# Optimization experiments

Measured on AMD Instinct MI355X. Metric: run time of the kernel, lower is better.

The kernel has to match this reference:

```python
import jax, jax.numpy as jnp
import numpy as np

N_HEAD = 4
GROUPS = 32
EPS = 1e-5


def _group_norm(x, w, b):
    B, C, H, W = x.shape
    g = x.reshape(B, GROUPS, C // GROUPS, H, W)
    mu = g.mean(axis=(2, 3, 4), keepdims=True)
    var = ((g - mu) ** 2).mean(axis=(2, 3, 4), keepdims=True)
    g = (g - mu) * jax.lax.rsqrt(var + EPS)
    return g.reshape(B, C, H, W) * w[None, :, None, None] + b[None, :, None, None]


def _l2norm(x):
    # F.normalize(x, dim=-1): x / max(||x||_2, 1e-12)
    n = jnp.sqrt(jnp.sum(x * x, axis=-1, keepdims=True))
    return x / jnp.maximum(n, 1e-12)


def _masked_softmax(attn, kk):
    # topk indices -> scatter 1s -> masked softmax (faithful to torch scatter_ path)
    idx = jax.lax.top_k(attn, kk)[1]                      # [B,H,c,kk]
    mask = jax.nn.one_hot(idx, attn.shape[-1], dtype=attn.dtype).sum(-2)  # [B,H,c,c]
    return jax.nn.softmax(jnp.where(mask > 0, attn, -jnp.inf), axis=-1)


def setup_inputs() -> dict:
    key = jax.random.key(0)
    ks = jax.random.split(key, 8)
    B, C, H, W = 4, 256, 128, 128
    x = jax.random.normal(ks[0], (B, C, H, W), jnp.float32)
    gn_w = 1.0 + 0.02 * jax.random.normal(ks[1], (C,), jnp.float32)
    gn_b = 0.02 * jax.random.normal(ks[2], (C,), jnp.float32)
    w_qkv = jax.random.normal(ks[3], (3 * C, C), jnp.float32) / np.sqrt(C).astype(np.float32)
    w_dw = jax.random.normal(ks[4], (3 * C, 1, 3, 3), jnp.float32) / 3.0
    w_out = jax.random.normal(ks[5], (C, C), jnp.float32) / np.sqrt(C).astype(np.float32)
    b_out = 0.01 * jax.random.normal(ks[6], (C,), jnp.float32)
    temperature = jnp.ones((N_HEAD, 1, 1), jnp.float32)
    attn_w = jnp.full((4,), 0.2, jnp.float32)  # attn1..attn4 combine weights
    return dict(x=x, gn_w=gn_w, gn_b=gn_b, w_qkv=w_qkv, w_dw=w_dw,
                w_out=w_out, b_out=b_out, temperature=temperature, attn_w=attn_w)


def reference(x, gn_w, gn_b, w_qkv, w_dw, w_out, b_out, temperature, attn_w):
    B, C, H, W = x.shape
    c = C // N_HEAD
    xn = _group_norm(x, gn_w, gn_b)
    # 1x1 conv (no bias)
    qkv = jnp.einsum('oi,bihw->bohw', w_qkv, xn)
    # 3x3 depthwise conv, padding=1, groups=3C, no bias
    qkv = jax.lax.conv_general_dilated(
        qkv, w_dw, window_strides=(1, 1), padding=((1, 1), (1, 1)),
        feature_group_count=3 * C,
        dimension_numbers=('NCHW', 'OIHW', 'NCHW'))
    q, k, v = jnp.split(qkv, 3, axis=1)
    # b (head c) h w -> b head c (h w)
    q = q.reshape(B, N_HEAD, c, H * W)
    k = k.reshape(B, N_HEAD, c, H * W)
    v = v.reshape(B, N_HEAD, c, H * W)
    q = _l2norm(q)
    k = _l2norm(k)
    # FFT cross-correlation attention (fftshift over ALL axes, as torch default)
    q_fft = jnp.fft.fftshift(jnp.fft.rfft2(q))   # [B,H,c,HW//2+1] complex
    k_fft = jnp.fft.fftshift(jnp.fft.rfft2(k))
    attn = jnp.einsum('bhcf,bhdf->bhcd', q_fft, k_fft) * temperature  # complex [B,H,c,c]
    attn = jnp.fft.irfft2(jnp.fft.ifftshift(attn), s=(c, c))          # real [B,H,c,c]
    ks_list = [c // 2, (c * 2) // 3, (c * 3) // 4, (c * 4) // 5]
    out = None
    for i, kk in enumerate(ks_list):
        a = _masked_softmax(attn, kk)
        o = jnp.einsum('bhcd,bhds->bhcs', a, v) * attn_w[i]
        out = o if out is None else out + o
    out = out.reshape(B, C, H, W)
    out = jnp.einsum('oi,bihw->bohw', w_out, out) + b_out[None, :, None, None]
    return out
```

## Files before the change

### kernel.cpp

```cpp
#include <hip/hip_runtime.h>
#include <math.h>

#define NC 256
#define CH3 768
#define HWSZ 16384

typedef __attribute__((ext_vector_type(8))) short short8;
typedef __attribute__((ext_vector_type(4))) float f32x4;
typedef __attribute__((ext_vector_type(4))) unsigned int u32x4;

static const size_t OFF_TW1   = 0;
static const size_t OFF_TW2   = 32768;
static const size_t OFF_HM    = 65536;
static const size_t OFF_SCALE = 65600;
static const size_t OFF_SHIFT = 66624;
static const size_t OFF_PACK  = 67648;
static const size_t OFF_AW    = 182336;
static const size_t OFF_GNP   = 444480;
static const size_t SHARED_END= 446528;

static const size_t R_QKV  = 0;
static const size_t R_SCR  = 12582912;
static const size_t R_H    = 25165824;
static const size_t R_PP   = 29360128;
static const size_t R_RP   = 30408704;
static const size_t R_ATTN = 31457280;
static const size_t R_ACOMB= 31473664;
static const size_t R_PS   = 31490048;
static const size_t R_RS   = 31506432;
static const size_t R_DWP  = 31522816;
static const size_t R_SSUM = 31532032;
static const size_t R_SALT = 31532800;
static const size_t R_SSQ  = 31533568;
static const size_t RSTRIDE= 31534336;
static const size_t HNOFF  = 8388608;

#define TDA_RH 0
#define TDA_RL 8192
#define TDA_IH 16384
#define TDA_IL 24576
#define ETA_RH 32768
#define ETA_RL 40960
#define ETA_IH 49152
#define ETA_IL 57344
#define STB_RH 65536
#define STB_RL 73728
#define STB_IH 81920
#define STB_IL 90112
#define STB_NIH 98304
#define STB_NIL 106496

#define AWQ_H 0
#define AWQ_L 98304
#define AWO_H 196608
#define AWO_L 229376

__device__ inline unsigned short b16rn(float x){
  unsigned u = __float_as_uint(x);
  return (unsigned short)((u + 0x7FFFu + ((u>>16)&1u)) >> 16);
}
__device__ inline unsigned int pk_hi(float x, float y){
  return (__float_as_uint(x)>>16) | (__float_as_uint(y) & 0xFFFF0000u);
}
__device__ inline unsigned int pk_lo(float x, float y){
  float xl = x - __uint_as_float(__float_as_uint(x) & 0xFFFF0000u);
  float yl = y - __uint_as_float(__float_as_uint(y) & 0xFFFF0000u);
  return (unsigned)b16rn(xl) | ((unsigned)b16rn(yl)<<16);
}
__device__ inline short8 ld8g(const unsigned int* p){ return *(const short8*)p; }
__device__ inline short8 ld8s(const unsigned short* p){ return *(const short8*)p; }
__device__ inline void wr_split(unsigned short* H, unsigned short* L, size_t o, float v){
  unsigned u = __float_as_uint(v);
  H[o] = (unsigned short)(u >> 16);
  L[o] = b16rn(v - __uint_as_float(u & 0xFFFF0000u));
}

__global__ __launch_bounds__(256) void init_tables_k(float* __restrict__ ws){
  int idx = blockIdx.x*256 + threadIdx.x;
  float2* tw1 = (float2*)(ws + OFF_TW1);
  float2* tw2 = (float2*)(ws + OFF_TW2);
  unsigned int* pk = (unsigned int*)(ws + OFF_PACK);
  const double P2 = 6.283185307179586476925286766559005;
  int m = idx >> 7, k = idx & 127;
  double a2 = P2 * (double)(m*k) / 16384.0;
  tw1[idx] = make_float2((float)cos(a2), (float)(-sin(a2)));
  tw2[idx] = make_float2((float)cos(a2), (float)( sin(a2)));
  if (idx < 64){
    double acc = 0.0;
    for (int v = 1; v < 32; v++) acc += sin(P2 * (double)((v*idx) & 63) / 64.0);
    ws[OFF_HM + idx] = (float)(-acc / 32.0);
  }
  if (idx < 8192){
    int r = idx >> 6, kp = idx & 63;
    int k0 = 2*kp, k1 = 2*kp+1;
    double a0 = P2 * (double)((r*k0) & 127) / 128.0;
    double a1 = P2 * (double)((r*k1) & 127) / 128.0;
    float c0 = (float)cos(a0), c1 = (float)cos(a1);
    float s0 = (float)sin(a0), s1 = (float)sin(a1);
    pk[TDA_RH + idx] = pk_hi(c0, c1);  pk[TDA_RL + idx] = pk_lo(c0, c1);
    pk[TDA_IH + idx] = pk_hi(-s0,-s1); pk[TDA_IL + idx] = pk_lo(-s0,-s1);
    pk[ETA_RH + idx] = pk_hi(c0, c1);  pk[ETA_RL + idx] = pk_lo(c0, c1);
    pk[ETA_IH + idx] = pk_hi(s0, s1);  pk[ETA_IL + idx] = pk_lo(s0, s1);
    float sr0, si0, sr1, si1;
    {
      int d0 = (r - k0) & 127, d1 = (r - k1) & 127;
      if (d0 == 0){ sr0 = 64.f; si0 = 0.f; }
      else if ((d0 & 1) == 0){ sr0 = 0.f; si0 = 0.f; }
      else { double th = 3.1415926535897932384626 * (double)d0 / 128.0;
             sr0 = 1.f; si0 = (float)(cos(th)/sin(th)); }
      if (d1 == 0){ sr1 = 64.f; si1 = 0.f; }
      else if ((d1 & 1) == 0){ sr1 = 0.f; si1 = 0.f; }
      else { double th = 3.1415926535897932384626 * (double)d1 / 128.0;
             sr1 = 1.f; si1 = (float)(cos(th)/sin(th)); }
    }
    pk[STB_RH + idx]  = pk_hi(sr0, sr1);  pk[STB_RL + idx]  = pk_lo(sr0, sr1);
    pk[STB_IH + idx]  = pk_hi(si0, si1);  pk[STB_IL + idx]  = pk_lo(si0, si1);
    pk[STB_NIH + idx] = pk_hi(-si0,-si1); pk[STB_NIL + idx] = pk_lo(-si0,-si1);
  }
}

__global__ __launch_bounds__(256) void wpack_k(const float* __restrict__ wqkv, const float* __restrict__ wout,
                                               unsigned int* __restrict__ aw){
  int id = blockIdx.x*256 + threadIdx.x;
  int row = id >> 7, kp = id & 127;
  if (row < CH3){
    float v0 = wqkv[row*256 + 2*kp], v1 = wqkv[row*256 + 2*kp + 1];
    aw[AWQ_H + row*128 + kp] = pk_hi(v0, v1);
    aw[AWQ_L + row*128 + kp] = pk_lo(v0, v1);
  } else {
    int r2 = row - CH3;
    float v0 = wout[r2*256 + 2*kp], v1 = wout[r2*256 + 2*kp + 1];
    aw[AWO_H + r2*128 + kp] = pk_hi(v0, v1);
    aw[AWO_L + r2*128 + kp] = pk_lo(v0, v1);
  }
}

__global__ __launch_bounds__(256) void gn_part_k(const float* __restrict__ x, float2* __restrict__ part){
  int id = blockIdx.x;
  const float4* p = (const float4*)(x + (size_t)id*HWSZ);
  int tid = threadIdx.x;
  float s = 0.f, sq = 0.f;
  #pragma unroll
  for (int i = 0; i < 16; i++){
    float4 v = p[tid + i*256];
    s  += v.x+v.y+v.z+v.w;
    sq += v.x*v.x+v.y*v.y+v.z*v.z+v.w*v.w;
  }
  __shared__ float r1[256], r2[256];
  r1[tid]=s; r2[tid]=sq; __syncthreads();
  for (int off=128; off; off>>=1){
    if (tid<off){ r1[tid]+=r1[tid+off]; r2[tid]+=r2[tid+off]; }
    __syncthreads();
  }
  if (tid==0) part[id] = make_float2(r1[0], r2[0]);
}
__global__ __launch_bounds__(128) void gn_fin_k(const float2* __restrict__ part, const float* __restrict__ gw,
                                                const float* __restrict__ gb, float* __restrict__ scale,
                                                float* __restrict__ shift){
  int bg = threadIdx.x;
  int b = bg >> 5, g = bg & 31;
  float s = 0.f, sq = 0.f;
  #pragma unroll
  for (int i = 0; i < 8; i++){
    float2 v = part[b*NC + g*8 + i];
    s += v.x; sq += v.y;
  }
  const float n = 8.0f*HWSZ;
  float mu = s/n, var = sq/n - mu*mu;
  float rs = rsqrtf(var + 1e-5f);
  for (int i = 0; i < 8; i++){
    int ch = g*8 + i;
    float sc = rs * gw[ch];
    scale[b*NC + ch] = sc;
    shift[b*NC + ch] = gb[ch] - mu*sc;
  }
}

__global__ __launch_bounds__(256) void packx_k(const float* __restrict__ xbase, const float* __restrict__ scale,
                                               const float* __restrict__ shift, float* __restrict__ R0,
                                               size_t rstride){
  int bz = blockIdx.z;
  const float* xb = xbase + (size_t)bz*NC*HWSZ;
  const float* sc = scale + bz*NC;
  const float* sh = shift + bz*NC;
  unsigned int* BqH = (unsigned int*)(R0 + (size_t)bz*rstride + R_H);
  unsigned int* BqL = BqH + 2097152;
  int kb = blockIdx.y;
  int n = blockIdx.x*256 + threadIdx.x;
  float v[8];
  #pragma unroll
  for (int c = 0; c < 8; c++){
    int ch = kb*8 + c;
    v[c] = xb[(size_t)ch*HWSZ + n]*sc[ch] + sh[ch];
  }
  u32x4 h, l;
  #pragma unroll
  for (int q = 0; q < 4; q++){
    h[q] = pk_hi(v[2*q], v[2*q+1]);
    l[q] = pk_lo(v[2*q], v[2*q+1]);
  }
  *(u32x4*)&BqH[((size_t)kb*HWSZ + n)*4] = h;
  *(u32x4*)&BqL[((size_t)kb*HWSZ + n)*4] = l;
}

__global__ __launch_bounds__(256) void gemm_pk(const unsigned int* __restrict__ Ah, const unsigned int* __restrict__ Al,
                                               const unsigned int* __restrict__ Bh0, const unsigned int* __restrict__ Bl0,
                                               const float* __restrict__ bias, float* __restrict__ C0,
                                               size_t bstride, size_t cstride){
  const unsigned int* Bh = Bh0 + (size_t)blockIdx.z*bstride;
  const unsigned int* Bl = Bl0 + (size_t)blockIdx.z*bstride;
  float* C = C0 + (size_t)blockIdx.z*cstride;
  int tid = threadIdx.x;
  int lane = tid & 63, wid = tid >> 6;
  int m0 = blockIdx.y*128, n0 = blockIdx.x*128;
  int wr = (wid>>1)*64, wc = (wid&1)*64;
  int lr = lane & 15, lk = lane >> 4;
  f32x4 acc[4][4] = {};
  size_t aoff[4], boff[4];
  #pragma unroll
  for (int i=0;i<4;i++) aoff[i] = (size_t)(m0 + wr + i*16 + lr)*128 + lk*4;
  #pragma unroll
  for (int j=0;j<4;j++) boff[j] = ((size_t)lk*HWSZ + n0 + wc + j*16 + lr)*4;
  short8 aH[2][4], aL[2][4], bH[2][4], bL[2][4];
  #pragma unroll
  for (int i=0;i<4;i++){ aH[0][i] = ld8g(Ah + aoff[i]); aL[0][i] = ld8g(Al + aoff[i]); }
  #pragma unroll
  for (int j=0;j<4;j++){ bH[0][j] = ld8g(Bh + boff[j]); bL[0][j] = ld8g(Bl + boff[j]); }
  #pragma unroll
  for (int kt = 0; kt < 8; kt++){
    int cur = kt & 1, nxt = cur ^ 1;
    if (kt < 7){
      size_t da = (size_t)(kt+1)*16;
      size_t db = (size_t)(kt+1)*4*HWSZ*4;
      #pragma unroll
      for (int i=0;i<4;i++){ aH[nxt][i] = ld8g(Ah + aoff[i] + da); aL[nxt][i] = ld8g(Al + aoff[i] + da); }
      #pragma unroll
      for (int j=0;j<4;j++){ bH[nxt][j] = ld8g(Bh + boff[j] + db); bL[nxt][j] = ld8g(Bl + boff[j] + db); }
    }
    #pragma unroll
    for (int i=0;i<4;i++)
      #pragma unroll
      for (int j=0;j<4;j++){
        acc[i][j] = __builtin_amdgcn_mfma_f32_16x16x32_bf16(aH[cur][i], bH[cur][j], acc[i][j], 0,0,0);
        acc[i][j] = __builtin_amdgcn_mfma_f32_16x16x32_bf16(aH[cur][i], bL[cur][j], acc[i][j], 0,0,0);
        acc[i][j] = __builtin_amdgcn_mfma_f32_16x16x32_bf16(aL[cur][i], bH[cur][j], acc[i][j], 0,0,0);
      }
  }
  #pragma unroll
  for (int i=0;i<4;i++){
    #pragma unroll
    for (int e=0;e<4;e++){
      int row = m0 + wr + i*16 + lk*4 + e;
      float bb = bias ? bias[row] : 0.0f;
      #pragma unroll
      for (int j=0;j<4;j++)
        C[(size_t)row*HWSZ + n0 + wc + j*16 + lr] = acc[i][j][e] + bb;
    }
  }
}

__global__ __launch_bounds__(256) void dwconv_tiled_k(float* __restrict__ R0, size_t rstride,
                                                      const float* __restrict__ wdw){
  float* Rb = R0 + (size_t)blockIdx.y*rstride;
  int blk = blockIdx.x;
  int ch = blk >> 2, sl = blk & 3;
  int h0 = sl*32;
  const float* in = Rb + R_SCR + (size_t)ch*HWSZ;
  float* part = Rb + R_DWP;
  float w[9];
  #pragma unroll
  for (int i=0;i<9;i++) w[i] = wdw[ch*9+i];
  __shared__ float tile[34][132];
  __shared__ float r0[256], r1[256], r2[256];
  int tid = threadIdx.x;
  #pragma unroll
  for (int i = 0; i < 5; i++){
    int id = tid + i*256;
    if (id < 1088){
      int r = id >> 5, c4 = id & 31;
      int gh = h0 - 1 + r;
      float4 v = (gh >= 0 && gh < 128) ? *(const float4*)&in[gh*128 + c4*4]
                                       : make_float4(0.f,0.f,0.f,0.f);
      *(float4*)&tile[r][c4*4] = v;
    }
  }
  __syncthreads();
  float s=0.f, sa=0.f, sq=0.f;
  #pragma unroll
  for (int it=0; it<4; it++){
    int idx = it*256 + tid;
    int lh = idx >> 5;
    int xq = idx & 31;
    int xb4 = xq*4;
    float o[4];
    #pragma unroll
    for (int e=0;e<4;e++){
      int xw = xb4 + e;
      float acc = 0.f;
      #pragma unroll
      for (int ky=0; ky<3; ky++){
        const float* tr = &tile[lh+ky][xw];
        if (xw > 0)   acc += tr[-1]*w[ky*3+0];
                      acc += tr[ 0]*w[ky*3+1];
        if (xw < 127) acc += tr[ 1]*w[ky*3+2];
      }
      o[e] = acc;
      s += acc; sq += acc*acc;
      sa += (e & 1) ? -acc : acc;
    }
    int sbase = (h0+lh)*128 + xb4;
    if (ch < 256){
      unsigned short* QHo = (unsigned short*)(Rb + R_QKV);
      unsigned short* QLo = (unsigned short*)(Rb + R_QKV + 2097152);
      size_t ro = (size_t)ch*HWSZ;
      #pragma unroll
      for (int e=0;e<4;e++){
        int sf = (16384 - (sbase+e)) & 16383;
        wr_split(QHo, QLo, ro + sf, o[e]);
      }
    } else if (ch < 512){
      unsigned short* KHo = (unsigned short*)(Rb + R_H);
      unsigned short* KLo = (unsigned short*)(Rb + R_H + 2097152);
      size_t ro = (size_t)(ch-256)*HWSZ;
      #pragma unroll
      for (int e=0;e<4;e++)
        wr_split(KHo, KLo, ro + sbase+e, o[e]);
    } else {
      *(float4*)&(Rb + R_QKV + (size_t)ch*HWSZ)[sbase] = make_float4(o[0],o[1],o[2],o[3]);
    }
  }
  r0[tid]=s; r1[tid]=sa; r2[tid]=sq; __syncthreads();
  for (int off=128; off; off>>=1){
    if (tid<off){ r0[tid]+=r0[tid+off]; r1[tid]+=r1[tid+off]; r2[tid]+=r2[tid+off]; }
    __syncthreads();
  }
  if (tid==0){ part[blk]=r0[0]; part[3072+blk]=r1[0]; part[6144+blk]=r2[0]; }
}

__global__ __launch_bounds__(256) void fft1_mfma_k(const float* __restrict__ ws, float* __restrict__ R0,
                                                   size_t rstride){
  float* Rb = R0 + (size_t)blockIdx.y*rstride;
  const unsigned short* KH = (const unsigned short*)(Rb + R_H);
  const unsigned short* KL = (const unsigned short*)(Rb + R_H + 2097152);
  float2* Tc = (float2*)(Rb + R_SCR);
  const unsigned int* PK = (const unsigned int*)(ws + OFF_PACK);
  const float2* tw1 = (const float2*)(ws + OFF_TW1);
  __shared__ unsigned int Bth[128][20], Btl[128][20];
  int tid = threadIdx.x;
  int lane = tid & 63, wid = tid >> 6;
  int wr = (wid>>1)*64, wc = (wid&1)*64;
  int lr = lane & 15, lk = lane >> 4;
  int row = blockIdx.x;
  f32x4 aR[4][4] = {}, aI[4][4] = {};
  int bc = tid & 127, grp = tid >> 7;
  for (int kt = 0; kt < 4; kt++){
    #pragma unroll
    for (int p=0;p<8;p++){
      int kp = grp*8 + p;
      int a = kt*32 + 2*kp;
      size_t o0 = (size_t)row*HWSZ + a*128 + bc;
      Bth[bc][kp] = (unsigned)KH[o0] | ((unsigned)KH[o0+128] << 16);
      Btl[bc][kp] = (unsigned)KL[o0] | ((unsigned)KL[o0+128] << 16);
    }
    __syncthreads();
    short8 bh[4], bl[4];
    #pragma unroll
    for (int j=0;j<4;j++){
      bh[j] = *(const short8*)&Bth[wc + j*16 + lr][lk*4];
      bl[j] = *(const short8*)&Btl[wc + j*16 + lr][lk*4];
    }
    #pragma unroll
    for (int i=0;i<4;i++){
      int off = (wr + i*16 + lr)*64 + kt*16 + lk*4;
      short8 ahR = ld8g(PK + TDA_RH + off), alR = ld8g(PK + TDA_RL + off);
      short8 ahI = ld8g(PK + TDA_IH + off), alI = ld8g(PK + TDA_IL + off);
      #pragma unroll
      for (int j=0;j<4;j++){
        aR[i][j] = __builtin_amdgcn_mfma_f32_16x16x32_bf16(ahR, bh[j], aR[i][j], 0,0,0);
        aR[i][j] = __builtin_amdgcn_mfma_f32_16x16x32_bf16(ahR, bl[j], aR[i][j], 0,0,0);
        aR[i][j] = __builtin_amdgcn_mfma_f32_16x16x32_bf16(alR, bh[j], aR[i][j], 0,0,0);
        aI[i][j] = __builtin_amdgcn_mfma_f32_16x16x32_bf16(ahI, bh[j], aI[i][j], 0,0,0);
        aI[i][j] = __builtin_amdgcn_mfma_f32_16x16x32_bf16(ahI, bl[j], aI[i][j], 0,0,0);
        aI[i][j] = __builtin_amdgcn_mfma_f32_16x16x32_bf16(alI, bh[j], aI[i][j], 0,0,0);
      }
    }
    __syncthreads();
  }
  #pragma unroll
  for (int i=0;i<4;i++)
    #pragma unroll
    for (int e=0;e<4;e++){
      int m = wr + i*16 + lk*4 + e;
      #pragma unroll
      for (int j=0;j<4;j++){
        int col = wc + j*16 + lr;
        float2 t = tw1[m*128 + col];
        float r = aR[i][j][e], im = aI[i][j][e];
        Tc[(size_t)m*32768 + row*128 + col] = make_float2(r*t.x - im*t.y, r*t.y + im*t.x);
      }
    }
}

__global__ __launch_bounds__(256) void fft2_mfma_k(const float* __restrict__ ws, float* __restrict__ R0,
                                                   size_t rstride){
  float* Rb = R0 + (size_t)blockIdx.y*rstride;
  float2* TU = (float2*)(Rb + R_SCR);
  const unsigned int* PK = (const unsigned int*)(ws + OFF_PACK);
  const float2* tw2 = (const float2*)(ws + OFF_TW2);
  __shared__ unsigned int ARh[128][20], ARl[128][20], AIh[128][20], AIl[128][20];
  int tid = threadIdx.x;
  int lane = tid & 63, wid = tid >> 6;
  int wr = (wid>>1)*64, wc = (wid&1)*64;
  int lr = lane & 15, lk = lane >> 4;
  int m0 = blockIdx.x*128;
  f32x4 aR[4][4] = {}, aI[4][4] = {};
  const float* Tf = (const float*)TU;
  for (int kt = 0; kt < 4; kt++){
    #pragma unroll
    for (int s=0;s<8;s++){
      int id = tid + s*256;
      int r = id >> 4, kp = id & 15;
      int k = kt*32 + 2*kp;
      float4 v = *(const float4*)&Tf[((size_t)(m0+r)*128 + k)*2];
      ARh[r][kp] = pk_hi(v.x, v.z); ARl[r][kp] = pk_lo(v.x, v.z);
      AIh[r][kp] = pk_hi(v.y, v.w); AIl[r][kp] = pk_lo(v.y, v.w);
    }
    __syncthreads();
    short8 ahR[4], alR[4], ahI[4], alI[4];
    #pragma unroll
    for (int i=0;i<4;i++){
      int ar = wr + i*16 + lr;
      ahR[i] = *(const short8*)&ARh[ar][lk*4];
      alR[i] = *(const short8*)&ARl[ar][lk*4];
      ahI[i] = *(const short8*)&AIh[ar][lk*4];
      alI[i] = *(const short8*)&AIl[ar][lk*4];
    }
    #pragma unroll
    for (int j=0;j<4;j++){
      int boff = (wc + j*16 + lr)*64 + kt*16 + lk*4;
      short8 bhR = ld8g(PK + STB_RH + boff), blR = ld8g(PK + STB_RL + boff);
      short8 bhI = ld8g(PK + STB_IH + boff), blI = ld8g(PK + STB_IL + boff);
      short8 bhN = ld8g(PK + STB_NIH + boff), blN = ld8g(PK + STB_NIL + boff);
      #pragma unroll
      for (int i=0;i<4;i++){
        aR[i][j] = __builtin_amdgcn_mfma_f32_16x16x32_bf16(ahR[i], bhR, aR[i][j], 0,0,0);
        aR[i][j] = __builtin_amdgcn_mfma_f32_16x16x32_bf16(ahR[i], blR, aR[i][j], 0,0,0);
        aR[i][j] = __builtin_amdgcn_mfma_f32_16x16x32_bf16(alR[i], bhR, aR[i][j], 0,0,0);
        aR[i][j] = __builtin_amdgcn_mfma_f32_16x16x32_bf16(ahI[i], bhN, aR[i][j], 0,0,0);
        aR[i][j] = __builtin_amdgcn_mfma_f32_16x16x32_bf16(ahI[i], blN, aR[i][j], 0,0,0);
        aR[i][j] = __builtin_amdgcn_mfma_f32_16x16x32_bf16(alI[i], bhN, aR[i][j], 0,0,0);
        aI[i][j] = __builtin_amdgcn_mfma_f32_16x16x32_bf16(ahR[i], bhI, aI[i][j], 0,0,0);
        aI[i][j] = __builtin_amdgcn_mfma_f32_16x16x32_bf16(ahR[i], blI, aI[i][j], 0,0,0);
        aI[i][j] = __builtin_amdgcn_mfma_f32_16x16x32_bf16(alR[i], bhI, aI[i][j], 0,0,0);
        aI[i][j] = __builtin_amdgcn_mfma_f32_16x16x32_bf16(ahI[i], bhR, aI[i][j], 0,0,0);
        aI[i][j] = __builtin_amdgcn_mfma_f32_16x16x32_bf16(ahI[i], blR, aI[i][j], 0,0,0);
        aI[i][j] = __builtin_amdgcn_mfma_f32_16x16x32_bf16(alI[i], bhR, aI[i][j], 0,0,0);
      }
    }
    __syncthreads();
  }
  #pragma unroll
  for (int i=0;i<4;i++)
    #pragma unroll
    for (int e=0;e<4;e++){
      int m = m0 + wr + i*16 + lk*4 + e;
      int f0 = m >> 8;
      #pragma unroll
      for (int j=0;j<4;j++){
        int col = wc + j*16 + lr;
        float2 t = tw2[f0*128 + col];
        float r = aR[i][j][e], im = aI[i][j][e];
        TU[(size_t)m*128 + col] = make_float2(r*t.x - im*t.y, r*t.y + im*t.x);
      }
    }
}

__global__ __launch_bounds__(256) void fft3_mfma_k(const float* __restrict__ ws, float* __restrict__ R0,
                                                   size_t rstride){
  float* Rb = R0 + (size_t)blockIdx.y*rstride;
  const float2* U = (const float2*)(Rb + R_SCR);
  unsigned short* HHo = (unsigned short*)(Rb + R_SCR + HNOFF);
  unsigned short* HLo = (unsigned short*)(Rb + R_SCR + HNOFF + 2097152);
  const unsigned int* PK = (const unsigned int*)(ws + OFF_PACK);
  __shared__ unsigned int BRh[128][20], BRl[128][20], BIh[128][20], BIl[128][20];
  int tid = threadIdx.x;
  int lane = tid & 63, wid = tid >> 6;
  int wr = (wid>>1)*64, wc = (wid&1)*64;
  int lr = lane & 15, lk = lane >> 4;
  int brow = blockIdx.x;
  f32x4 ac[4][4] = {};
  int bc = tid & 127, grp = tid >> 7;
  for (int kt = 0; kt < 4; kt++){
    #pragma unroll
    for (int p=0;p<8;p++){
      int kp = grp*8 + p;
      int k = kt*32 + 2*kp;
      float2 v0 = U[((size_t)k*256 + brow)*128 + bc];
      float2 v1 = U[((size_t)(k+1)*256 + brow)*128 + bc];
      BRh[bc][kp] = pk_hi(v0.x, v1.x); BRl[bc][kp] = pk_lo(v0.x, v1.x);
      BIh[bc][kp] = pk_hi(v0.y, v1.y); BIl[bc][kp] = pk_lo(v0.y, v1.y);
    }
    __syncthreads();
    short8 ahR[4], alR[4], ahI[4], alI[4];
    #pragma unroll
    for (int i=0;i<4;i++){
      int off = (wr + i*16 + lr)*64 + kt*16 + lk*4;
      ahR[i] = ld8g(PK + ETA_RH + off); alR[i] = ld8g(PK + ETA_RL + off);
      ahI[i] = ld8g(PK + ETA_IH + off); alI[i] = ld8g(PK + ETA_IL + off);
    }
    #pragma unroll
    for (int j=0;j<4;j++){
      int col = wc + j*16 + lr;
      short8 bhR = *(const short8*)&BRh[col][lk*4];
      short8 blR = *(const short8*)&BRl[col][lk*4];
      short8 bhI = *(const short8*)&BIh[col][lk*4];
      short8 blI = *(const short8*)&BIl[col][lk*4];
      #pragma unroll
      for (int i=0;i<4;i++){
        ac[i][j] = __builtin_amdgcn_mfma_f32_16x16x32_bf16(ahR[i], bhI, ac[i][j], 0,0,0);
        ac[i][j] = __builtin_amdgcn_mfma_f32_16x16x32_bf16(ahR[i], blI, ac[i][j], 0,0,0);
        ac[i][j] = __builtin_amdgcn_mfma_f32_16x16x32_bf16(alR[i], bhI, ac[i][j], 0,0,0);
        ac[i][j] = __builtin_amdgcn_mfma_f32_16x16x32_bf16(ahI[i], bhR, ac[i][j], 0,0,0);
        ac[i][j] = __builtin_amdgcn_mfma_f32_16x16x32_bf16(ahI[i], blR, ac[i][j], 0,0,0);
        ac[i][j] = __builtin_amdgcn_mfma_f32_16x16x32_bf16(alI[i], bhR, ac[i][j], 0,0,0);
      }
    }
    __syncthreads();
  }
  #pragma unroll
  for (int i=0;i<4;i++)
    #pragma unroll
    for (int e=0;e<4;e++){
      int m = wr + i*16 + lk*4 + e;
      #pragma unroll
      for (int j=0;j<4;j++){
        int col = wc + j*16 + lr;
        float v = ac[i][j][e];
        unsigned u = __float_as_uint(v);
        size_t o = (size_t)brow*HWSZ + m*128 + col;
        HHo[o] = (unsigned short)(u >> 16);
        HLo[o] = b16rn(v - __uint_as_float(u & 0xFFFF0000u));
      }
    }
}

__global__ __launch_bounds__(256) void pri3_k(float* __restrict__ R0, size_t rstride){
  float* Rb = R0 + (size_t)blockIdx.z*rstride;
  int sp = blockIdx.x, head = blockIdx.y;
  const unsigned short* QH = (const unsigned short*)(Rb + R_QKV);
  const unsigned short* QL = (const unsigned short*)(Rb + R_QKV + 2097152);
  const unsigned short* KH = (const unsigned short*)(Rb + R_H);
  const unsigned short* KL = (const unsigned short*)(Rb + R_H + 2097152);
  const unsigned short* HNH = (const unsigned short*)(Rb + R_SCR + HNOFF);
  const unsigned short* HNL = HNH + 2097152*2;
  float* Pp = Rb + R_PP;
  float* Rp = Rb + R_RP;
  int tid = threadIdx.x, lane = tid & 63, wid = tid >> 6;
  int wr = (wid>>1)*32, wc = (wid&1)*32;
  int lr = lane & 15, lk = lane >> 4;
  size_t qoff[2], koff[2];
  #pragma unroll
  for (int i=0;i<2;i++) qoff[i] = (size_t)(head*64 + wr + i*16 + lr)*HWSZ + sp*256 + lk*8;
  #pragma unroll
  for (int j=0;j<2;j++) koff[j] = (size_t)(head*64 + wc + j*16 + lr)*HWSZ + sp*256 + lk*8;
  f32x4 aP[2][2] = {}, aRi[2][2] = {};
  short8 qh[2][2], ql[2][2], k1h[2][2], k1l[2][2], k2h[2][2], k2l[2][2];
#define LDPRI(B,T) { int d = (T)*32; \
    _Pragma("unroll") \
    for (int i=0;i<2;i++){ \
      qh[B][i] = ld8s(QH + qoff[i] + d); \
      ql[B][i] = ld8s(QL + qoff[i] + d); } \
    _Pragma("unroll") \
    for (int j=0;j<2;j++){ \
      k1h[B][j] = ld8s(KH + koff[j] + d); \
      k1l[B][j] = ld8s(KL + koff[j] + d); \
      k2h[B][j] = ld8s(HNH + koff[j] + d); \
      k2l[B][j] = ld8s(HNL + koff[j] + d); } }
  LDPRI(0,0);
  #pragma unroll
  for (int kt = 0; kt < 8; kt++){
    int cur = kt & 1;
    if (kt < 7) LDPRI(cur^1, kt+1);
    #pragma unroll
    for (int i=0;i<2;i++)
      #pragma unroll
      for (int j=0;j<2;j++){
        aP[i][j]  = __builtin_amdgcn_mfma_f32_16x16x32_bf16(qh[cur][i], k1h[cur][j], aP[i][j], 0,0,0);
        aP[i][j]  = __builtin_amdgcn_mfma_f32_16x16x32_bf16(qh[cur][i], k1l[cur][j], aP[i][j], 0,0,0);
        aP[i][j]  = __builtin_amdgcn_mfma_f32_16x16x32_bf16(ql[cur][i], k1h[cur][j], aP[i][j], 0,0,0);
        aRi[i][j] = __builtin_amdgcn_mfma_f32_16x16x32_bf16(qh[cur][i], k2h[cur][j], aRi[i][j], 0,0,0);
        aRi[i][j] = __builtin_amdgcn_mfma_f32_16x16x32_bf16(qh[cur][i], k2l[cur][j], aRi[i][j], 0,0,0);
        aRi[i][j] = __builtin_amdgcn_mfma_f32_16x16x32_bf16(ql[cur][i], k2h[cur][j], aRi[i][j], 0,0,0);
      }
  }
#undef LDPRI
  size_t obase = ((size_t)(sp*4 + head)) << 12;
  #pragma unroll
  for (int i=0;i<2;i++)
    #pragma unroll
    for (int e=0;e<4;e++){
      int row = wr + i*16 + lk*4 + e;
      #pragma unroll
      for (int j=0;j<2;j++){
        int col = wc + j*16 + lr;
        size_t o = obase + (size_t)row*64 + col;
        Pp[o] = aP[i][j][e];
        Rp[o] = aRi[i][j][e];
      }
    }
}

__global__ __launch_bounds__(256) void red_k(float* __restrict__ R0, size_t rstride){
  float* Rb = R0 + (size_t)blockIdx.y*rstride;
  const float* Pp = Rb + R_PP;
  const float* Rp = Rb + R_RP;
  float* Ps = Rb + R_PS;
  float* Rs = Rb + R_RS;
  int tid = threadIdx.x;
  #pragma unroll
  for (int rep=0; rep<2; rep++){
    int g = blockIdx.x*512 + rep*256 + tid;
    int head = g >> 12, loc = g & 4095;
    float p = 0.f, ri = 0.f;
    for (int sp=0; sp<64; sp++){
      size_t o = ((size_t)(sp*4+head)<<12) + loc;
      p += Pp[o]; ri += Rp[o];
    }
    Ps[g] = p; Rs[g] = ri;
  }
  if (blockIdx.x == 0){
    const float* part = Rb + R_DWP;
    for (int ch = tid; ch < CH3; ch += 256){
      float s=0.f, sa=0.f, sq=0.f;
      #pragma unroll
      for (int sl=0; sl<4; sl++){
        s  += part[ch*4+sl];
        sa += part[3072+ch*4+sl];
        sq += part[6144+ch*4+sl];
      }
      Rb[R_SSUM+ch]=s; Rb[R_SALT+ch]=sa; Rb[R_SSQ+ch]=sq;
    }
  }
}

__global__ __launch_bounds__(256) void attn_build_k(const float* __restrict__ ws, float* __restrict__ R0,
                                                    size_t rstride, const float* __restrict__ temperature){
  float* Rb = R0 + (size_t)blockIdx.y*rstride;
  const float* Ps   = Rb + R_PS;
  const float* Rs   = Rb + R_RS;
  const float* ssum = Rb + R_SSUM;
  const float* salt = Rb + R_SALT;
  const float* ssq  = Rb + R_SSQ;
  float* attn = Rb + R_ATTN;
  const float* hmg  = ws + OFF_HM;
  __shared__ float Rn[64][65], Ril[64][65], hm[64];
  int head = blockIdx.x;
  int tid = threadIdx.x;
  if (tid < 64) hm[tid] = hmg[tid];
  for (int t=0;t<16;t++){
    int idx = tid + t*256; int c = idx>>6, d = idx&63;
    float P = Ps[head*4096 + idx], Ri = Rs[head*4096 + idx];
    int qch = head*64 + c;
    int kch = 256 + head*64 + d;
    float qs=ssum[qch], qa=salt[qch], qn=fmaxf(sqrtf(ssq[qch]), 1e-12f);
    float ks=ssum[kch], ka=salt[kch], kn=fmaxf(sqrtf(ssq[kch]), 1e-12f);
    float Rr = 0.5f*(16384.0f*P + qs*ks + qa*ka);
    float sc = 1.0f/(qn*kn);
    Rn[c][d]  = Rr*sc;
    Ril[c][d] = Ri*sc;
  }
  __syncthreads();
  float tmp2 = temperature[(head+2)&3];
  for (int t=0;t<16;t++){
    int idx = tid + t*256; int c = idx>>6, e = idx&63;
    float s = Rn[c][e];
    #pragma unroll 8
    for (int d=0; d<64; d++) s += Ril[c][d]*hm[(e-d)&63];
    attn[((size_t)head<<12) + (size_t)(c*64+e)] = s*tmp2;
  }
}

__global__ __launch_bounds__(64) void topk_k(float* __restrict__ R0, size_t rstride,
                                             const float* __restrict__ attn_w){
  float* Rb = R0 + (size_t)blockIdx.y*rstride;
  const float* attn = Rb + R_ATTN;
  float* Acomb = Rb + R_ACOMB;
  int blk = blockIdx.x;
  int tid = threadIdx.x;
  __shared__ float row[64];
  float v = attn[(size_t)blk*64 + tid];
  row[tid] = v;
  __syncthreads();
  int rank = 0; float vmax = -1e30f;
  for (int l=0;l<64;l++){
    float w = row[l];
    if (w > v || (w == v && l < tid)) rank++;
    vmax = fmaxf(vmax, w);
  }
  float e = expf(v - vmax);
  const int kks[4] = {32,42,48,51};
  float denom[4];
  #pragma unroll
  for (int i=0;i<4;i++){
    float x = (rank < kks[i]) ? e : 0.0f;
    #pragma unroll
    for (int off=32; off; off>>=1) x += __shfl_xor(x, off);
    denom[i] = x;
  }
  float wgt = 0.f;
  #pragma unroll
  for (int i=0;i<4;i++) if (rank < kks[i]) wgt += attn_w[i] / denom[i];
  Acomb[(size_t)blk*64 + tid] = e * wgt;
}

__global__ __launch_bounds__(256) void av_k(float* __restrict__ R0, size_t rstride){
  float* Rb = R0 + (size_t)blockIdx.z*rstride;
  const float* Acomb = Rb + R_ACOMB;
  unsigned int* BqH = (unsigned int*)(Rb + R_H);
  unsigned int* BqL = BqH + 2097152;
  int head = blockIdx.y;
  int n0 = blockIdx.x*64;
  const float* Vb = Rb + R_QKV + (size_t)(512 + head*64)*HWSZ;
  __shared__ float As[64][65], Bs[16][65];
  int tid=threadIdx.x, tx=tid&15, ty=tid>>4;
  for (int t=0;t<16;t++){ int idx=tid+t*256; As[idx>>6][idx&63] = Acomb[((size_t)head<<12)+idx]; }
  __syncthreads();
  float acc[4][4]={};
  for (int k0=0;k0<64;k0+=16){
    #pragma unroll
    for (int i=0;i<4;i++){ int id=tid+i*256; int nn=id&63, k=id>>6;
      Bs[k][nn] = Vb[(size_t)(k0+k)*HWSZ + n0+nn]; }
    __syncthreads();
    #pragma unroll
    for (int k=0;k<16;k++){
      float a[4], bv[4];
      #pragma unroll
      for (int i=0;i<4;i++) a[i]=As[ty*4+i][k0+k];
      #pragma unroll
      for (int j=0;j<4;j++) bv[j]=Bs[k][tx*4+j];
      #pragma unroll
      for (int i=0;i<4;i++)
        #pragma unroll
        for (int j=0;j<4;j++) acc[i][j] += a[i]*bv[j];
    }
    __syncthreads();
  }
  int kpa = head*32 + ty*2;
  int kba = kpa >> 2, qa = kpa & 3;
  int kpb = kpa + 1;
  int kbb = kpb >> 2, qb = kpb & 3;
  #pragma unroll
  for (int j=0;j<4;j++){
    int n = n0 + tx*4 + j;
    BqH[((size_t)kba*HWSZ + n)*4 + qa] = pk_hi(acc[0][j], acc[1][j]);
    BqL[((size_t)kba*HWSZ + n)*4 + qa] = pk_lo(acc[0][j], acc[1][j]);
    BqH[((size_t)kbb*HWSZ + n)*4 + qb] = pk_hi(acc[2][j], acc[3][j]);
    BqL[((size_t)kbb*HWSZ + n)*4 + qb] = pk_lo(acc[2][j], acc[3][j]);
  }
}

extern "C" void kernel_launch(void* const* d_in, const int* in_sizes, int n_in,
                              void* d_out, int out_size, void* d_ws, size_t ws_size,
                              hipStream_t stream) {
  const float* x     = (const float*)d_in[0];
  const float* gn_w  = (const float*)d_in[1];
  const float* gn_b  = (const float*)d_in[2];
  const float* w_qkv = (const float*)d_in[3];
  const float* w_dw  = (const float*)d_in[4];
  const float* w_out = (const float*)d_in[5];
  const float* b_out = (const float*)d_in[6];
  const float* temperature = (const float*)d_in[7];
  const float* attn_w = (const float*)d_in[8];
  float* out = (float*)d_out;
  float* ws  = (float*)d_ws;
  unsigned int* AW = (unsigned int*)(ws + OFF_AW);
  float* R0 = ws + SHARED_END;
  const size_t CHW = (size_t)NC*HWSZ;

  size_t need2 = (SHARED_END + 2*RSTRIDE)*sizeof(float);
  size_t need4 = (SHARED_END + 4*RSTRIDE)*sizeof(float);
  int zb = (ws_size >= need4) ? 4 : (ws_size >= need2) ? 2 : 1;

  init_tables_k<<<64,256,0,stream>>>(ws);
  wpack_k<<<512,256,0,stream>>>(w_qkv, w_out, AW);
  gn_part_k<<<1024,256,0,stream>>>(x, (float2*)(ws+OFF_GNP));
  gn_fin_k<<<1,128,0,stream>>>((const float2*)(ws+OFF_GNP), gn_w, gn_b,
                               ws+OFF_SCALE, ws+OFF_SHIFT);

  for (int b0 = 0; b0 < 4; b0 += zb){
    packx_k<<<dim3(64,32,zb),256,0,stream>>>(x + (size_t)b0*CHW, ws+OFF_SCALE+b0*NC,
                                             ws+OFF_SHIFT+b0*NC, R0, RSTRIDE);
    gemm_pk<<<dim3(128,6,zb),256,0,stream>>>(AW+AWQ_H, AW+AWQ_L,
                                             (unsigned int*)(R0+R_H), (unsigned int*)(R0+R_H)+2097152,
                                             nullptr, R0+R_SCR, RSTRIDE, RSTRIDE);
    dwconv_tiled_k<<<dim3(3072,zb),256,0,stream>>>(R0, RSTRIDE, w_dw);
    fft1_mfma_k<<<dim3(256,zb),256,0,stream>>>(ws, R0, RSTRIDE);
    fft2_mfma_k<<<dim3(256,zb),256,0,stream>>>(ws, R0, RSTRIDE);
    fft3_mfma_k<<<dim3(256,zb),256,0,stream>>>(ws, R0, RSTRIDE);
    pri3_k<<<dim3(64,4,zb),256,0,stream>>>(R0, RSTRIDE);
    red_k<<<dim3(32,zb),256,0,stream>>>(R0, RSTRIDE);
    attn_build_k<<<dim3(4,zb),256,0,stream>>>(ws, R0, RSTRIDE, temperature);
    topk_k<<<dim3(256,zb),64,0,stream>>>(R0, RSTRIDE, attn_w);
    av_k<<<dim3(256,4,zb),256,0,stream>>>(R0, RSTRIDE);
    gemm_pk<<<dim3(128,2,zb),256,0,stream>>>(AW+AWO_H, AW+AWO_L,
                                             (unsigned int*)(R0+R_H), (unsigned int*)(R0+R_H)+2097152,
                                             b_out, out + (size_t)b0*CHW, RSTRIDE, CHW);
  }
}
```

Measured before the change: 810.4 us.

## Store FFT intermediates as split bf16 planes and drop LDS staging in fft2

fft1 and fft2 now write their twiddled outputs as four separate bf16 hi/lo planes (real and imaginary) instead of interleaved float2. fft2 reads its A operands straight from global memory in MFMA fragment layout, which removes the LDS staging and barriers, and it launches twice as many blocks with half the rows each. fft3 reads the split planes directly. The intent is to cut intermediate traffic and conversion work and to raise occupancy. The trade-off is more scattered 16-bit global accesses and repeated B-fragment loads across the extra blocks.

```diff
diff --git a/kernel.cpp b/kernel.cpp
--- a/kernel.cpp
+++ b/kernel.cpp
@@ -342,7 +342,10 @@
   float* Rb = R0 + (size_t)blockIdx.y*rstride;
   const unsigned short* KH = (const unsigned short*)(Rb + R_H);
   const unsigned short* KL = (const unsigned short*)(Rb + R_H + 2097152);
-  float2* Tc = (float2*)(Rb + R_SCR);
+  unsigned short* TRH = (unsigned short*)(Rb + R_SCR);
+  unsigned short* TRL = TRH + 4194304;
+  unsigned short* TIH = TRL + 4194304;
+  unsigned short* TIL = TIH + 4194304;
   const unsigned int* PK = (const unsigned int*)(ws + OFF_PACK);
   const float2* tw1 = (const float2*)(ws + OFF_TW1);
   __shared__ unsigned int Bth[128][20], Btl[128][20];
@@ -396,7 +399,10 @@
         int col = wc + j*16 + lr;
         float2 t = tw1[m*128 + col];
         float r = aR[i][j][e], im = aI[i][j][e];
-        Tc[(size_t)m*32768 + row*128 + col] = make_float2(r*t.x - im*t.y, r*t.y + im*t.x);
+        float vr = r*t.x - im*t.y, vi = r*t.y + im*t.x;
+        size_t o = (size_t)m*32768 + row*128 + col;
+        wr_split(TRH, TRL, o, vr);
+        wr_split(TIH, TIL, o, vi);
       }
     }
 }
@@ -404,45 +410,37 @@
 __global__ __launch_bounds__(256) void fft2_mfma_k(const float* __restrict__ ws, float* __restrict__ R0,
                                                    size_t rstride){
   float* Rb = R0 + (size_t)blockIdx.y*rstride;
-  float2* TU = (float2*)(Rb + R_SCR);
+  unsigned short* TRH = (unsigned short*)(Rb + R_SCR);
+  unsigned short* TRL = TRH + 4194304;
+  unsigned short* TIH = TRL + 4194304;
+  unsigned short* TIL = TIH + 4194304;
   const unsigned int* PK = (const unsigned int*)(ws + OFF_PACK);
   const float2* tw2 = (const float2*)(ws + OFF_TW2);
-  __shared__ unsigned int ARh[128][20], ARl[128][20], AIh[128][20], AIl[128][20];
-  int tid = threadIdx.x;
-  int lane = tid & 63, wid = tid >> 6;
-  int wr = (wid>>1)*64, wc = (wid&1)*64;
+  int tid = threadIdx.x, lane = tid & 63, wid = tid >> 6;
+  int row = blockIdx.x >> 1, mh = blockIdx.x & 1;
+  int wr1 = (wid>>1)*32, wc1 = (wid&1)*64;
   int lr = lane & 15, lk = lane >> 4;
-  int m0 = blockIdx.x*128;
-  f32x4 aR[4][4] = {}, aI[4][4] = {};
-  const float* Tf = (const float*)TU;
+  f32x4 aR[2][4] = {}, aI[2][4] = {};
+  size_t aoff[2];
+  #pragma unroll
+  for (int i=0;i<2;i++) aoff[i] = (size_t)(mh*64 + wr1 + i*16 + lr)*32768 + (size_t)row*128 + lk*8;
+  #pragma unroll
   for (int kt = 0; kt < 4; kt++){
-    #pragma unroll
-    for (int s=0;s<8;s++){
-      int id = tid + s*256;
-      int r = id >> 4, kp = id & 15;
-      int k = kt*32 + 2*kp;
-      float4 v = *(const float4*)&Tf[((size_t)(m0+r)*128 + k)*2];
-      ARh[r][kp] = pk_hi(v.x, v.z); ARl[r][kp] = pk_lo(v.x, v.z);
-      AIh[r][kp] = pk_hi(v.y, v.w); AIl[r][kp] = pk_lo(v.y, v.w);
-    }
-    __syncthreads();
-    short8 ahR[4], alR[4], ahI[4], alI[4];
-    #pragma unroll
-    for (int i=0;i<4;i++){
-      int ar = wr + i*16 + lr;
-      ahR[i] = *(const short8*)&ARh[ar][lk*4];
-      alR[i] = *(const short8*)&ARl[ar][lk*4];
-      ahI[i] = *(const short8*)&AIh[ar][lk*4];
-      alI[i] = *(const short8*)&AIl[ar][lk*4];
+    short8 ahR[2], alR[2], ahI[2], alI[2];
+    #pragma unroll
+    for (int i=0;i<2;i++){
+      size_t o = aoff[i] + kt*32;
+      ahR[i] = ld8s(TRH + o); alR[i] = ld8s(TRL + o);
+      ahI[i] = ld8s(TIH + o); alI[i] = ld8s(TIL + o);
     }
     #pragma unroll
     for (int j=0;j<4;j++){
-      int boff = (wc + j*16 + lr)*64 + kt*16 + lk*4;
+      int boff = (wc1 + j*16 + lr)*64 + kt*16 + lk*4;
       short8 bhR = ld8g(PK + STB_RH + boff), blR = ld8g(PK + STB_RL + boff);
       short8 bhI = ld8g(PK + STB_IH + boff), blI = ld8g(PK + STB_IL + boff);
       short8 bhN = ld8g(PK + STB_NIH + boff), blN = ld8g(PK + STB_NIL + boff);
       #pragma unroll
-      for (int i=0;i<4;i++){
+      for (int i=0;i<2;i++){
         aR[i][j] = __builtin_amdgcn_mfma_f32_16x16x32_bf16(ahR[i], bhR, aR[i][j], 0,0,0);
         aR[i][j] = __builtin_amdgcn_mfma_f32_16x16x32_bf16(ahR[i], blR, aR[i][j], 0,0,0);
         aR[i][j] = __builtin_amdgcn_mfma_f32_16x16x32_bf16(alR[i], bhR, aR[i][j], 0,0,0);
@@ -457,28 +455,33 @@
         aI[i][j] = __builtin_amdgcn_mfma_f32_16x16x32_bf16(alI[i], bhR, aI[i][j], 0,0,0);
       }
     }
-    __syncthreads();
-  }
-  #pragma unroll
-  for (int i=0;i<4;i++)
-    #pragma unroll
-    for (int e=0;e<4;e++){
-      int m = m0 + wr + i*16 + lk*4 + e;
-      int f0 = m >> 8;
-      #pragma unroll
-      for (int j=0;j<4;j++){
-        int col = wc + j*16 + lr;
-        float2 t = tw2[f0*128 + col];
-        float r = aR[i][j][e], im = aI[i][j][e];
-        TU[(size_t)m*128 + col] = make_float2(r*t.x - im*t.y, r*t.y + im*t.x);
-      }
-    }
+  }
+  #pragma unroll
+  for (int i=0;i<2;i++){
+    int f0b = mh*64 + wr1 + i*16 + lk*4;
+    #pragma unroll
+    for (int j=0;j<4;j++){
+      int r = wc1 + j*16 + lr;
+      #pragma unroll
+      for (int e=0;e<4;e++){
+        float2 t = tw2[(f0b+e)*128 + r];
+        float rr = aR[i][j][e], ii = aI[i][j][e];
+        float ur = rr*t.x - ii*t.y, ui = rr*t.y + ii*t.x;
+        size_t o = (size_t)(f0b+e)*32768 + (size_t)row*128 + r;
+        wr_split(TRH, TRL, o, ur);
+        wr_split(TIH, TIL, o, ui);
+      }
+    }
+  }
 }
 
 __global__ __launch_bounds__(256) void fft3_mfma_k(const float* __restrict__ ws, float* __restrict__ R0,
                                                    size_t rstride){
   float* Rb = R0 + (size_t)blockIdx.y*rstride;
-  const float2* U = (const float2*)(Rb + R_SCR);
+  const unsigned short* URH = (const unsigned short*)(Rb + R_SCR);
+  const unsigned short* URL = URH + 4194304;
+  const unsigned short* UIH = URL + 4194304;
+  const unsigned short* UIL = UIH + 4194304;
   unsigned short* HHo = (unsigned short*)(Rb + R_SCR + HNOFF);
   unsigned short* HLo = (unsigned short*)(Rb + R_SCR + HNOFF + 2097152);
   const unsigned int* PK = (const unsigned int*)(ws + OFF_PACK);
@@ -495,10 +498,11 @@
     for (int p=0;p<8;p++){
       int kp = grp*8 + p;
       int k = kt*32 + 2*kp;
-      float2 v0 = U[((size_t)k*256 + brow)*128 + bc];
-      float2 v1 = U[((size_t)(k+1)*256 + brow)*128 + bc];
-      BRh[bc][kp] = pk_hi(v0.x, v1.x); BRl[bc][kp] = pk_lo(v0.x, v1.x);
-      BIh[bc][kp] = pk_hi(v0.y, v1.y); BIl[bc][kp] = pk_lo(v0.y, v1.y);
+      size_t o0 = (size_t)k*32768 + (size_t)brow*128 + bc;
+      BRh[bc][kp] = (unsigned)URH[o0] | ((unsigned)URH[o0+32768] << 16);
+      BRl[bc][kp] = (unsigned)URL[o0] | ((unsigned)URL[o0+32768] << 16);
+      BIh[bc][kp] = (unsigned)UIH[o0] | ((unsigned)UIH[o0+32768] << 16);
+      BIl[bc][kp] = (unsigned)UIL[o0] | ((unsigned)UIL[o0+32768] << 16);
     }
     __syncthreads();
     short8 ahR[4], alR[4], ahI[4], alI[4];
@@ -795,7 +799,7 @@
                                              nullptr, R0+R_SCR, RSTRIDE, RSTRIDE);
     dwconv_tiled_k<<<dim3(3072,zb),256,0,stream>>>(R0, RSTRIDE, w_dw);
     fft1_mfma_k<<<dim3(256,zb),256,0,stream>>>(ws, R0, RSTRIDE);
-    fft2_mfma_k<<<dim3(256,zb),256,0,stream>>>(ws, R0, RSTRIDE);
+    fft2_mfma_k<<<dim3(512,zb),256,0,stream>>>(ws, R0, RSTRIDE);
     fft3_mfma_k<<<dim3(256,zb),256,0,stream>>>(ws, R0, RSTRIDE);
     pri3_k<<<dim3(64,4,zb),256,0,stream>>>(R0, RSTRIDE);
     red_k<<<dim3(32,zb),256,0,stream>>>(R0, RSTRIDE);
```

Measured after the change: 906.2 us. +11.8%, slower.
